# Performance work log

Measured on AMD Instinct MI355X. Metric: run time of the kernel, lower is better.

The kernel has to match this reference:

```python
import jax, jax.numpy as jnp
import numpy as np

N_HEADS = 16
N_KV_HEADS = 4
WINDOW = 128
THETA = 10000.0


def _rope_cos_sin(T, half):
    inv = 1.0 / (THETA ** (jnp.arange(half, dtype=jnp.float32) / half))
    f = jnp.arange(T, dtype=jnp.float32)[:, None] * inv[None, :]  # (T, half)
    return jnp.cos(f), jnp.sin(f)


def _apply_rope(x, cos, sin):
    # x: (B, H, T, hd); interleaved (real, imag) pairs like torch view_as_complex
    xr, xi = x[..., 0::2], x[..., 1::2]
    out_r = xr * cos - xi * sin
    out_i = xr * sin + xi * cos
    return jnp.stack([out_r, out_i], axis=-1).reshape(x.shape)


def setup_inputs() -> dict:
    key = jax.random.key(0)
    ks = jax.random.split(key, 6)
    B, T, C = 1, 4096, 2048
    kvC = (C // N_HEADS) * N_KV_HEADS
    return {
        "x": jax.random.normal(ks[0], (B, T, C), dtype=jnp.float32),
        "wq": jax.random.normal(ks[1], (C, C), dtype=jnp.float32) * 0.02,
        "wk": jax.random.normal(ks[2], (C, kvC), dtype=jnp.float32) * 0.02,
        "wv": jax.random.normal(ks[3], (C, kvC), dtype=jnp.float32) * 0.02,
        "wo": jax.random.normal(ks[4], (C, C), dtype=jnp.float32) * 0.02,
        "sink": jnp.zeros((1, N_HEADS, 1, 1), dtype=jnp.float32),
    }


def reference(x, wq, wk, wv, wo, sink):
    B, T, C = x.shape
    hd = C // N_HEADS
    n_rep = N_HEADS // N_KV_HEADS

    q = (x @ wq).reshape(B, T, N_HEADS, hd).transpose(0, 2, 1, 3)    # (B,H,T,hd)
    k = (x @ wk).reshape(B, T, N_KV_HEADS, hd).transpose(0, 2, 1, 3)  # (B,Hkv,T,hd)
    v = (x @ wv).reshape(B, T, N_KV_HEADS, hd).transpose(0, 2, 1, 3)

    cos, sin = _rope_cos_sin(T, hd // 2)  # (T, hd/2), broadcasts over (B,H,T,hd/2)
    q = _apply_rope(q, cos, sin)
    k = _apply_rope(k, cos, sin)

    # GQA head expansion (repeat_interleave over head dim)
    k = jnp.repeat(k, n_rep, axis=1)
    v = jnp.repeat(v, n_rep, axis=1)

    att = jnp.einsum("bhqd,bhkd->bhqk", q, k) * (hd ** -0.5) + sink

    # symmetric sliding-window band: |i - j| <= window//2
    idx = jnp.arange(T)
    band = jnp.abs(idx[:, None] - idx[None, :]) <= (WINDOW // 2)
    att = jnp.where(band[None, None, :, :], att, -jnp.inf)

    att = jax.nn.softmax(att, axis=-1)
    # torch code replaces NaN rows (fully-masked) with uniform; band always has diag so no-op
    att = jnp.where(jnp.isnan(att), 1.0 / T, att)

    out = jnp.einsum("bhqk,bhkd->bqhd", att, v).reshape(B, T, C)
    return out @ wo
```

## Files before the change

### kernel.cpp

```cpp
#include <hip/hip_runtime.h>
#include <stdint.h>

#define T_SEQ 4096
#define C_DIM 2048
#define HD 128

typedef unsigned short ushort_t;
typedef __attribute__((ext_vector_type(8))) short shortx8;
typedef __attribute__((ext_vector_type(4))) float floatx4;
typedef __attribute__((ext_vector_type(8))) unsigned short u16x8;
typedef __attribute__((ext_vector_type(4))) unsigned short u16x4;

__device__ __forceinline__ ushort_t f2bf(float f) {
  union { float f; uint32_t u; } v; v.f = f;
  v.u += 0x7fffu + ((v.u >> 16) & 1u);
  return (ushort_t)(v.u >> 16);
}
__device__ __forceinline__ void load_lds16(const ushort_t* g, ushort_t* l) {
  __builtin_amdgcn_global_load_lds(
      (const __attribute__((address_space(1))) unsigned int*)g,
      (__attribute__((address_space(3))) unsigned int*)l, 16, 0, 0);
}

__global__ __launch_bounds__(256) void prep_kernel(
    const float* __restrict__ wq, const float* __restrict__ wk,
    const float* __restrict__ wv, const float* __restrict__ wo,
    const float* __restrict__ x,
    ushort_t* __restrict__ BtAll, ushort_t* __restrict__ woT,
    ushort_t* __restrict__ xb) {
  const int bid = blockIdx.x;
  const int tid = threadIdx.x;
  if (bid >= 2560) {
    int i = (bid - 2560) * 256 + tid;
    float4 v = ((const float4*)x)[i];
    u16x4 o; o[0] = f2bf(v.x); o[1] = f2bf(v.y); o[2] = f2bf(v.z); o[3] = f2bf(v.w);
    ((u16x4*)xb)[i] = o;
    return;
  }
  const float* src; ushort_t* dst; int C, bx, by;
  if (bid < 1024) { src = wq; dst = BtAll; C = 2048; bx = bid & 31; by = bid >> 5; }
  else if (bid < 1280) { int b = bid - 1024; src = wk; dst = BtAll + (size_t)2048 * 2048; C = 512; bx = b & 7; by = b >> 3; }
  else if (bid < 1536) { int b = bid - 1280; src = wv; dst = BtAll + (size_t)2560 * 2048; C = 512; bx = b & 7; by = b >> 3; }
  else { int b = bid - 1536; src = wo; dst = woT; C = 2048; bx = b & 31; by = b >> 5; }
  const int R = 2048;

  __shared__ float tile[64][65];
  const int c0 = bx * 64, r0 = by * 64;
  for (int i = tid; i < 1024; i += 256) {
    int r = i >> 4, cc = (i & 15) * 4;
    float4 v = *(const float4*)&src[(size_t)(r0 + r) * C + c0 + cc];
    tile[r][cc] = v.x; tile[r][cc + 1] = v.y; tile[r][cc + 2] = v.z; tile[r][cc + 3] = v.w;
  }
  __syncthreads();
  for (int i = tid; i < 512; i += 256) {
    int oc = i >> 3;
    int g = (i & 7) * 8;
    u16x8 o;
    for (int j = 0; j < 8; ++j) o[j] = f2bf(tile[g + j][oc]);
    *(u16x8*)&dst[(size_t)(c0 + oc) * R + r0 + g] = o;
  }
}

struct GemmAcc { floatx4 a[4][4]; };

__device__ __forceinline__ void gemm_core_bk64(
    const ushort_t* __restrict__ A, const ushort_t* __restrict__ Bt,
    ushort_t* As, ushort_t* Bs, GemmAcc& acc,
    int m0, int n0, int K, int tid, int lane, int wave, int quad, int l16,
    int wm, int wn) {
  const int nk = K >> 6;
  for (int kk = 0; kk < nk; ++kk) {
    const int k0 = kk << 6;
    for (int r = 0; r < 4; ++r) {
      int e = r * 256 + tid;
      int row = e >> 3;
      int p = e & 7;
      int g = (p - row) & 7;
      const ushort_t* ga = A + (size_t)(m0 + row) * K + k0 + g * 8;
      const ushort_t* gb = Bt + (size_t)(n0 + row) * K + k0 + g * 8;
      ushort_t* la = As + (size_t)(r * 256 + (tid & 192)) * 8;
      ushort_t* lb = Bs + (size_t)(r * 256 + (tid & 192)) * 8;
      load_lds16(ga, la);
      load_lds16(gb, lb);
    }
    __syncthreads();
    for (int ks = 0; ks < 2; ++ks) {
      shortx8 af[4], bfr[4];
      for (int i = 0; i < 4; ++i) {
        int ar = wm + i * 16 + l16;
        af[i] = *(const shortx8*)(As + ar * 64 + (((ks << 2) + quad + ar) & 7) * 8);
        int br = wn + i * 16 + l16;
        bfr[i] = *(const shortx8*)(Bs + br * 64 + (((ks << 2) + quad + br) & 7) * 8);
      }
      for (int i = 0; i < 4; ++i)
        for (int j = 0; j < 4; ++j)
          acc.a[i][j] = __builtin_amdgcn_mfma_f32_16x16x32_bf16(af[i], bfr[j], acc.a[i][j], 0, 0, 0);
    }
    __syncthreads();
  }
}

__global__ __launch_bounds__(256, 3) void gemm_bf16(
    const ushort_t* __restrict__ A, const ushort_t* __restrict__ Bt,
    float* __restrict__ C, int M, int N, int K) {
  __shared__ __align__(16) ushort_t As[128 * 64];
  __shared__ __align__(16) ushort_t Bs[128 * 64];
  const int tid = threadIdx.x;
  const int lane = tid & 63;
  const int wave = tid >> 6;
  const int quad = lane >> 4;
  const int l16 = lane & 15;
  const int m0 = blockIdx.y * 128;
  const int n0 = blockIdx.x * 128;
  const int wm = (wave & 1) * 64;
  const int wn = (wave >> 1) * 64;

  GemmAcc acc = {};
  gemm_core_bk64(A, Bt, As, Bs, acc, m0, n0, K, tid, lane, wave, quad, l16, wm, wn);

  for (int i = 0; i < 4; ++i)
    for (int j = 0; j < 4; ++j) {
      int col = n0 + wn + j * 16 + l16;
      int rbase = m0 + wm + i * 16 + quad * 4;
      for (int r = 0; r < 4; ++r)
        C[(size_t)(rbase + r) * N + col] = acc.a[i][j][r];
    }
}

#define BARF() do { __builtin_amdgcn_s_barrier(); asm volatile("" ::: "memory"); } while (0)

__global__ __launch_bounds__(512, 2) void gemm_qkv256(
    const ushort_t* __restrict__ A, const ushort_t* __restrict__ Bt,
    ushort_t* __restrict__ qbb, ushort_t* __restrict__ kbb,
    ushort_t* __restrict__ vtb) {
  __shared__ __align__(16) ushort_t SA[2][16384];
  __shared__ __align__(16) ushort_t SB[2][16384];
  const int tid = threadIdx.x;
  const int lane = tid & 63;
  const int w = tid >> 6;
  const int l16 = lane & 15;
  const int quad = lane >> 4;
  const int wm = (w >> 2) * 128;
  const int wn = (w & 3) * 64;
  const int aq = wm + (w & 3) * 16;
  const int bq = wn + (w >> 2) * 16;
  const int gl8 = lane >> 3;
  const int gch = ((lane & 7) - gl8) & 7;

  const int bid = blockIdx.x;
  const int swz = (bid & 7) * 24 + (bid >> 3);
  const int n0 = (swz % 12) * 256;
  const int m0 = (swz / 12) * 256;

  const int off0 = l16 * 64 + ((quad + l16) & 7) * 8;
  const int off1 = l16 * 64 + ((4 + quad + l16) & 7) * 8;

  floatx4 acc[8][4] = {};
  shortx8 a0k0[4], a0k1[4], a1k0[4], a1k1[4];
  shortx8 b0k0[2], b0k1[2], b1k0[2], b1k1[2];

  auto issue2 = [&](const ushort_t* __restrict__ G, int gRow, ushort_t* L, int r0, int k0) {
#pragma unroll
    for (int u = 0; u < 2; ++u) {
      const ushort_t* src = G + (size_t)(gRow + r0 + u * 8 + gl8) * 2048 + k0 + gch * 8;
      load_lds16(src, L + (r0 + u * 8) * 64);
    }
  };

#define LOAD_A(base, Sb, D0, D1)                                  \
  _Pragma("unroll")                                               \
  for (int i2 = 0; i2 < 4; ++i2) {                                \
    const int rb = (wm + ((base) + i2) * 16) * 64;                \
    D0[i2] = *(const shortx8*)&(Sb)[rb + off0];                   \
    D1[i2] = *(const shortx8*)&(Sb)[rb + off1];                   \
  }
#define LOAD_B(jb, Sb, D0, D1)                                    \
  _Pragma("unroll")                                               \
  for (int j2 = 0; j2 < 2; ++j2) {                                \
    const int rb = (wn + ((jb) + j2) * 16) * 64;                  \
    D0[j2] = *(const shortx8*)&(Sb)[rb + off0];                   \
    D1[j2] = *(const shortx8*)&(Sb)[rb + off1];                   \
  }
#define MFMA16(ih, jh, A0, A1, B0, B1)                            \
  __builtin_amdgcn_s_setprio(1);                                  \
  _Pragma("unroll")                                               \
  for (int i2 = 0; i2 < 4; ++i2)                                  \
    _Pragma("unroll")                                             \
    for (int j2 = 0; j2 < 2; ++j2) {                              \
      acc[(ih)*4+i2][(jh)*2+j2] = __builtin_amdgcn_mfma_f32_16x16x32_bf16( \
          A0[i2], B0[j2], acc[(ih)*4+i2][(jh)*2+j2], 0, 0, 0);    \
      acc[(ih)*4+i2][(jh)*2+j2] = __builtin_amdgcn_mfma_f32_16x16x32_bf16( \
          A1[i2], B1[j2], acc[(ih)*4+i2][(jh)*2+j2], 0, 0, 0);    \
    }                                                             \
  __builtin_amdgcn_s_setprio(0);

  issue2(A, m0, SA[0], aq, 0);        issue2(A, m0, SA[0], aq + 64, 0);
  issue2(Bt, n0, SB[0], bq, 0);       issue2(Bt, n0, SB[0], bq + 32, 0);
  issue2(A, m0, SA[1], aq + 64, 64);  issue2(Bt, n0, SB[1], bq + 32, 64);
  asm volatile("s_waitcnt vmcnt(4)" ::: "memory");
  BARF();

  for (int t2 = 0; t2 < 16; ++t2) {
#pragma unroll
    for (int half = 0; half < 2; ++half) {
      const int t = t2 * 2 + half;
      ushort_t* SAb = SA[half];
      ushort_t* SBb = SB[half];
      ushort_t* SAo = SA[half ^ 1];
      ushort_t* SBo = SB[half ^ 1];

      LOAD_A(0, SAb, a0k0, a0k1);
      LOAD_B(0, SBb, b0k0, b0k1);
      LOAD_B(2, SBb, b1k0, b1k1);
      if (t + 1 < 32) issue2(A, m0, SAo, aq, (t + 1) * 64);
      BARF();
      MFMA16(0, 0, a0k0, a0k1, b0k0, b0k1);
      BARF();

      LOAD_A(4, SAb, a1k0, a1k1);
      if (t + 1 < 32) issue2(Bt, n0, SBo, bq, (t + 1) * 64);
      BARF();
      MFMA16(0, 1, a0k0, a0k1, b1k0, b1k1);
      BARF();

      if (t + 2 < 32) issue2(Bt, n0, SBb, bq + 32, (t + 2) * 64);
      BARF();
      MFMA16(1, 1, a1k0, a1k1, b1k0, b1k1);
      BARF();

      if (t + 2 < 32) issue2(A, m0, SAb, aq + 64, (t + 2) * 64);
      BARF();
      MFMA16(1, 0, a1k0, a1k1, b0k0, b0k1);
      if (t < 30)       { asm volatile("s_waitcnt vmcnt(4)" ::: "memory"); }
      else if (t == 30) { asm volatile("s_waitcnt vmcnt(0)" ::: "memory"); }
      BARF();
    }
  }

  asm volatile("s_waitcnt vmcnt(0) lgkmcnt(0)" ::: "memory");
  BARF();

  if (n0 < 2560) {
    const bool isq = (n0 < 2048);
    const int par = l16 & 1;
#pragma unroll
    for (int j = 0; j < 4; ++j) {
      int col = n0 + wn + j * 16 + l16;
      int irot = (col & 127) >> 1;
      float inv = __expf(-0.14391157f * (float)irot);
#pragma unroll
      for (int i = 0; i < 8; ++i) {
        int t0r = m0 + wm + i * 16 + quad * 4;
#pragma unroll
        for (int r = 0; r < 4; ++r) {
          float val = acc[i][j][r];
          float other = __shfl_xor(val, 1, 64);
          float sn, cs;
          __sincosf((float)(t0r + r) * inv, &sn, &cs);
          float outv = par ? (other * sn + val * cs) : (val * cs - other * sn);
          if (isq) qbb[(size_t)(t0r + r) * 2048 + col] = f2bf(outv);
          else     kbb[(size_t)(t0r + r) * 512 + (col - 2048)] = f2bf(outv);
        }
      }
    }
  } else {
#pragma unroll
    for (int j = 0; j < 4; ++j) {
      int dim = n0 + wn + j * 16 + l16 - 2560;
#pragma unroll
      for (int i = 0; i < 8; ++i) {
        int t0r = m0 + wm + i * 16 + quad * 4;
        u16x4 o;
#pragma unroll
        for (int r = 0; r < 4; ++r) o[r] = f2bf(acc[i][j][r]);
        *(u16x4*)&vtb[(size_t)dim * T_SEQ + t0r] = o;
      }
    }
  }
#undef LOAD_A
#undef LOAD_B
#undef MFMA16
}

#define LSTR 168
__global__ __launch_bounds__(512, 1) void attn_kernel(
    const ushort_t* __restrict__ qbb, const ushort_t* __restrict__ kbb,
    const ushort_t* __restrict__ vtb, ushort_t* __restrict__ ao) {
  __shared__ __align__(16) ushort_t QP[128 * LSTR];
  __shared__ __align__(16) ushort_t KV[160 * LSTR];

  const int tid = threadIdx.x;
  const int lane = tid & 63;
  const int wave = tid >> 6;
  const int l16 = lane & 15;
  const int quad = lane >> 4;
  const int kvh = blockIdx.x;
  const int h0 = kvh * 4;
  const int t0 = blockIdx.y * 32;
  const int kstart = t0 - 64;
  const int hsel = wave & 3;
  const int qh = wave >> 2;
  const float scale = 0.08838834764831845f;

  for (int c = tid; c < 2048; c += 512) {
    int row = c >> 4, c8 = c & 15;
    int h = h0 + (row >> 5);
    int q = t0 + (row & 31);
    u16x8 v = *(const u16x8*)&qbb[(size_t)q * C_DIM + h * HD + c8 * 8];
    *(u16x8*)&QP[row * LSTR + c8 * 8] = v;
  }
  for (int c = tid; c < 2560; c += 512) {
    int row = c >> 4, c8 = c & 15;
    int t = kstart + row;
    u16x8 v;
    if (t >= 0 && t < T_SEQ) {
      v = *(const u16x8*)&kbb[(size_t)t * 512 + kvh * HD + c8 * 8];
    } else {
      for (int z = 0; z < 8; ++z) v[z] = 0;
    }
    *(u16x8*)&KV[row * LSTR + c8 * 8] = v;
  }
  __syncthreads();

  floatx4 acc[10] = {};
  const int arow = hsel * 32 + qh * 16 + l16;
  for (int ks = 0; ks < 4; ++ks) {
    shortx8 af = *(const shortx8*)&QP[arow * LSTR + ks * 32 + quad * 8];
    for (int kt = 0; kt < 10; ++kt) {
      shortx8 bf = *(const shortx8*)&KV[(kt * 16 + l16) * LSTR + ks * 32 + quad * 8];
      acc[kt] = __builtin_amdgcn_mfma_f32_16x16x32_bf16(af, bf, acc[kt], 0, 0, 0);
    }
  }

  float mrow[4] = {-3e38f, -3e38f, -3e38f, -3e38f};
  for (int kt = 0; kt < 10; ++kt) {
    int col = kt * 16 + l16;
    int kg = kstart + col;
    for (int r = 0; r < 4; ++r) {
      int row = qh * 16 + quad * 4 + r;
      bool valid = (kg >= 0) && (kg < T_SEQ) && (col >= row) && (col <= row + 128);
      float s = valid ? acc[kt][r] * scale : -3e38f;
      acc[kt][r] = s;
      mrow[r] = fmaxf(mrow[r], s);
    }
  }
  for (int off = 1; off < 16; off <<= 1)
    for (int r = 0; r < 4; ++r)
      mrow[r] = fmaxf(mrow[r], __shfl_xor(mrow[r], off, 64));
  float rl[4];
  for (int r = 0; r < 4; ++r) {
    float s = 0.f;
    for (int kt = 0; kt < 10; ++kt) {
      float p = __expf(acc[kt][r] - mrow[r]);
      acc[kt][r] = p;
      s += p;
    }
    rl[r] = s;
  }
  for (int off = 1; off < 16; off <<= 1)
    for (int r = 0; r < 4; ++r) rl[r] += __shfl_xor(rl[r], off, 64);
  for (int r = 0; r < 4; ++r) rl[r] = 1.0f / rl[r];

  __syncthreads();

  for (int kt = 0; kt < 10; ++kt) {
    int col = kt * 16 + l16;
    for (int r = 0; r < 4; ++r) {
      int row = hsel * 32 + qh * 16 + quad * 4 + r;
      QP[row * LSTR + col] = f2bf(acc[kt][r] * rl[r]);
    }
  }
  for (int c = tid; c < 2560; c += 512) {
    int dim = c / 20, c8 = c % 20;
    int k0 = kstart + c8 * 8;
    const ushort_t* g = &vtb[(size_t)(kvh * HD + dim) * T_SEQ];
    u16x8 v;
    if (k0 >= 0 && k0 + 7 < T_SEQ) {
      v = *(const u16x8*)&g[k0];
    } else {
      for (int z = 0; z < 8; ++z) {
        int kk = k0 + z;
        v[z] = (kk >= 0 && kk < T_SEQ) ? g[kk] : (ushort_t)0;
      }
    }
    *(u16x8*)&KV[dim * LSTR + c8 * 8] = v;
  }
  __syncthreads();

  floatx4 oacc[8] = {};
  const int prow = hsel * 32 + qh * 16 + l16;
  for (int ks = 0; ks < 5; ++ks) {
    shortx8 pf = *(const shortx8*)&QP[prow * LSTR + ks * 32 + quad * 8];
    for (int dt = 0; dt < 8; ++dt) {
      shortx8 vf = *(const shortx8*)&KV[(dt * 16 + l16) * LSTR + ks * 32 + quad * 8];
      oacc[dt] = __builtin_amdgcn_mfma_f32_16x16x32_bf16(pf, vf, oacc[dt], 0, 0, 0);
    }
  }

  const int h = h0 + hsel;
  for (int r = 0; r < 4; ++r) {
    int row = t0 + qh * 16 + quad * 4 + r;
    for (int dt = 0; dt < 8; ++dt) {
      int dim = dt * 16 + l16;
      ao[(size_t)row * C_DIM + h * HD + dim] = f2bf(oacc[dt][r]);
    }
  }
}

extern "C" void kernel_launch(void* const* d_in, const int* in_sizes, int n_in,
                              void* d_out, int out_size, void* d_ws, size_t ws_size,
                              hipStream_t stream) {
  const float* x  = (const float*)d_in[0];
  const float* wq = (const float*)d_in[1];
  const float* wk = (const float*)d_in[2];
  const float* wv = (const float*)d_in[3];
  const float* wo = (const float*)d_in[4];
  float* out = (float*)d_out;

  char* ws = (char*)d_ws;
  ushort_t* BtAll = (ushort_t*)(ws);
  ushort_t* woT   = (ushort_t*)(ws + 12582912);
  ushort_t* xb    = (ushort_t*)(ws + 20971520);
  ushort_t* qbb   = (ushort_t*)(ws + 37748736);
  ushort_t* kbb   = (ushort_t*)(ws + 54525952);
  ushort_t* vtb   = (ushort_t*)(ws + 58720256);
  ushort_t* ao    = (ushort_t*)(ws + 62914560);

  prep_kernel<<<10752, 256, 0, stream>>>(wq, wk, wv, wo, x, BtAll, woT, xb);

  gemm_qkv256<<<192, 512, 0, stream>>>(xb, BtAll, qbb, kbb, vtb);

  attn_kernel<<<dim3(4, 128), 512, 0, stream>>>(qbb, kbb, vtb, ao);

  gemm_bf16<<<dim3(16, 32), 256, 0, stream>>>(ao, woT, out, 4096, 2048, 2048);
}
```

Baseline: 256.6 us.

## Double query tile per attention block to reuse K/V window loads

The attention kernel now handles 64 query positions per block instead of 32. Each wave processes two 16-row query sub-tiles against a 208-row K/V window, and the grid is halved. The intent is to cut redundant loads of the overlapping K/V window, since the 128-key halo is amortized over twice as many queries. This costs more LDS, more registers per wave from the doubled accumulators, and fewer blocks for parallelism. The QKV GEMM's launch bound minimum-blocks hint also changes from 2 to 1, which may loosen register limits.

```diff
diff --git a/kernel.cpp b/kernel.cpp
--- a/kernel.cpp
+++ b/kernel.cpp
@@ -129,7 +129,7 @@
 
 #define BARF() do { __builtin_amdgcn_s_barrier(); asm volatile("" ::: "memory"); } while (0)
 
-__global__ __launch_bounds__(512, 2) void gemm_qkv256(
+__global__ __launch_bounds__(512, 1) void gemm_qkv256(
     const ushort_t* __restrict__ A, const ushort_t* __restrict__ Bt,
     ushort_t* __restrict__ qbb, ushort_t* __restrict__ kbb,
     ushort_t* __restrict__ vtb) {
@@ -282,12 +282,14 @@
 #undef MFMA16
 }
 
-#define LSTR 168
+#define QSTR 168
+#define KSTR 168
+#define VSTR 216
 __global__ __launch_bounds__(512, 1) void attn_kernel(
     const ushort_t* __restrict__ qbb, const ushort_t* __restrict__ kbb,
     const ushort_t* __restrict__ vtb, ushort_t* __restrict__ ao) {
-  __shared__ __align__(16) ushort_t QP[128 * LSTR];
-  __shared__ __align__(16) ushort_t KV[160 * LSTR];
+  __shared__ __align__(16) ushort_t QP[256 * QSTR];
+  __shared__ __align__(16) ushort_t KV[208 * KSTR];
 
   const int tid = threadIdx.x;
   const int lane = tid & 63;
@@ -296,20 +298,20 @@
   const int quad = lane >> 4;
   const int kvh = blockIdx.x;
   const int h0 = kvh * 4;
-  const int t0 = blockIdx.y * 32;
+  const int t0 = blockIdx.y * 64;
   const int kstart = t0 - 64;
   const int hsel = wave & 3;
   const int qh = wave >> 2;
   const float scale = 0.08838834764831845f;
 
-  for (int c = tid; c < 2048; c += 512) {
+  for (int c = tid; c < 4096; c += 512) {
     int row = c >> 4, c8 = c & 15;
-    int h = h0 + (row >> 5);
-    int q = t0 + (row & 31);
+    int h = h0 + (row >> 6);
+    int q = t0 + (row & 63);
     u16x8 v = *(const u16x8*)&qbb[(size_t)q * C_DIM + h * HD + c8 * 8];
-    *(u16x8*)&QP[row * LSTR + c8 * 8] = v;
-  }
-  for (int c = tid; c < 2560; c += 512) {
+    *(u16x8*)&QP[row * QSTR + c8 * 8] = v;
+  }
+  for (int c = tid; c < 3328; c += 512) {
     int row = c >> 4, c8 = c & 15;
     int t = kstart + row;
     u16x8 v;
@@ -318,60 +320,77 @@
     } else {
       for (int z = 0; z < 8; ++z) v[z] = 0;
     }
-    *(u16x8*)&KV[row * LSTR + c8 * 8] = v;
+    *(u16x8*)&KV[row * KSTR + c8 * 8] = v;
   }
   __syncthreads();
 
-  floatx4 acc[10] = {};
-  const int arow = hsel * 32 + qh * 16 + l16;
+  const int qb0 = qh * 32, qb1 = qb0 + 16;
+  const int tb0 = qb0 >> 4, tb1 = tb0 + 1;
+  floatx4 acc0[10] = {}, acc1[10] = {};
   for (int ks = 0; ks < 4; ++ks) {
-    shortx8 af = *(const shortx8*)&QP[arow * LSTR + ks * 32 + quad * 8];
+    shortx8 af0 = *(const shortx8*)&QP[(hsel * 64 + qb0 + l16) * QSTR + ks * 32 + quad * 8];
+    shortx8 af1 = *(const shortx8*)&QP[(hsel * 64 + qb1 + l16) * QSTR + ks * 32 + quad * 8];
     for (int kt = 0; kt < 10; ++kt) {
-      shortx8 bf = *(const shortx8*)&KV[(kt * 16 + l16) * LSTR + ks * 32 + quad * 8];
-      acc[kt] = __builtin_amdgcn_mfma_f32_16x16x32_bf16(af, bf, acc[kt], 0, 0, 0);
-    }
-  }
-
-  float mrow[4] = {-3e38f, -3e38f, -3e38f, -3e38f};
-  for (int kt = 0; kt < 10; ++kt) {
-    int col = kt * 16 + l16;
-    int kg = kstart + col;
+      shortx8 bf0 = *(const shortx8*)&KV[((tb0 + kt) * 16 + l16) * KSTR + ks * 32 + quad * 8];
+      acc0[kt] = __builtin_amdgcn_mfma_f32_16x16x32_bf16(af0, bf0, acc0[kt], 0, 0, 0);
+      shortx8 bf1 = *(const shortx8*)&KV[((tb1 + kt) * 16 + l16) * KSTR + ks * 32 + quad * 8];
+      acc1[kt] = __builtin_amdgcn_mfma_f32_16x16x32_bf16(af1, bf1, acc1[kt], 0, 0, 0);
+    }
+  }
+
+  float rl0[4], rl1[4];
+#pragma unroll
+  for (int s = 0; s < 2; ++s) {
+    floatx4* acc = s ? acc1 : acc0;
+    const int qb = s ? qb1 : qb0;
+    const int tb = s ? tb1 : tb0;
+    float* rl = s ? rl1 : rl0;
+    float mrow[4] = {-3e38f, -3e38f, -3e38f, -3e38f};
+    for (int kt = 0; kt < 10; ++kt) {
+      int col = (tb + kt) * 16 + l16;
+      int kg = kstart + col;
+      for (int r = 0; r < 4; ++r) {
+        int qrow = qb + quad * 4 + r;
+        bool valid = (kg >= 0) && (kg < T_SEQ) && (col >= qrow) && (col <= qrow + 128);
+        float sc = valid ? acc[kt][r] * scale : -3e38f;
+        acc[kt][r] = sc;
+        mrow[r] = fmaxf(mrow[r], sc);
+      }
+    }
+    for (int off = 1; off < 16; off <<= 1)
+      for (int r = 0; r < 4; ++r)
+        mrow[r] = fmaxf(mrow[r], __shfl_xor(mrow[r], off, 64));
     for (int r = 0; r < 4; ++r) {
-      int row = qh * 16 + quad * 4 + r;
-      bool valid = (kg >= 0) && (kg < T_SEQ) && (col >= row) && (col <= row + 128);
-      float s = valid ? acc[kt][r] * scale : -3e38f;
-      acc[kt][r] = s;
-      mrow[r] = fmaxf(mrow[r], s);
-    }
-  }
-  for (int off = 1; off < 16; off <<= 1)
-    for (int r = 0; r < 4; ++r)
-      mrow[r] = fmaxf(mrow[r], __shfl_xor(mrow[r], off, 64));
-  float rl[4];
-  for (int r = 0; r < 4; ++r) {
-    float s = 0.f;
+      float ss = 0.f;
+      for (int kt = 0; kt < 10; ++kt) {
+        float p = __expf(acc[kt][r] - mrow[r]);
+        acc[kt][r] = p;
+        ss += p;
+      }
+      rl[r] = ss;
+    }
+    for (int off = 1; off < 16; off <<= 1)
+      for (int r = 0; r < 4; ++r) rl[r] += __shfl_xor(rl[r], off, 64);
+    for (int r = 0; r < 4; ++r) rl[r] = 1.0f / rl[r];
+  }
+
+  __syncthreads();
+
+#pragma unroll
+  for (int s = 0; s < 2; ++s) {
+    floatx4* acc = s ? acc1 : acc0;
+    const int qb = s ? qb1 : qb0;
+    float* rl = s ? rl1 : rl0;
     for (int kt = 0; kt < 10; ++kt) {
-      float p = __expf(acc[kt][r] - mrow[r]);
-      acc[kt][r] = p;
-      s += p;
-    }
-    rl[r] = s;
-  }
-  for (int off = 1; off < 16; off <<= 1)
-    for (int r = 0; r < 4; ++r) rl[r] += __shfl_xor(rl[r], off, 64);
-  for (int r = 0; r < 4; ++r) rl[r] = 1.0f / rl[r];
-
-  __syncthreads();
-
-  for (int kt = 0; kt < 10; ++kt) {
-    int col = kt * 16 + l16;
-    for (int r = 0; r < 4; ++r) {
-      int row = hsel * 32 + qh * 16 + quad * 4 + r;
-      QP[row * LSTR + col] = f2bf(acc[kt][r] * rl[r]);
-    }
-  }
-  for (int c = tid; c < 2560; c += 512) {
-    int dim = c / 20, c8 = c % 20;
+      int col = kt * 16 + l16;
+      for (int r = 0; r < 4; ++r) {
+        int row = hsel * 64 + qb + quad * 4 + r;
+        QP[row * QSTR + col] = f2bf(acc[kt][r] * rl[r]);
+      }
+    }
+  }
+  for (int c = tid; c < 3328; c += 512) {
+    int dim = c / 26, c8 = c % 26;
     int k0 = kstart + c8 * 8;
     const ushort_t* g = &vtb[(size_t)(kvh * HD + dim) * T_SEQ];
     u16x8 v;
@@ -383,26 +402,29 @@
         v[z] = (kk >= 0 && kk < T_SEQ) ? g[kk] : (ushort_t)0;
       }
     }
-    *(u16x8*)&KV[dim * LSTR + c8 * 8] = v;
+    *(u16x8*)&KV[dim * VSTR + c8 * 8] = v;
   }
   __syncthreads();
 
-  floatx4 oacc[8] = {};
-  const int prow = hsel * 32 + qh * 16 + l16;
-  for (int ks = 0; ks < 5; ++ks) {
-    shortx8 pf = *(const shortx8*)&QP[prow * LSTR + ks * 32 + quad * 8];
-    for (int dt = 0; dt < 8; ++dt) {
-      shortx8 vf = *(const shortx8*)&KV[(dt * 16 + l16) * LSTR + ks * 32 + quad * 8];
-      oacc[dt] = __builtin_amdgcn_mfma_f32_16x16x32_bf16(pf, vf, oacc[dt], 0, 0, 0);
-    }
-  }
-
-  const int h = h0 + hsel;
-  for (int r = 0; r < 4; ++r) {
-    int row = t0 + qh * 16 + quad * 4 + r;
-    for (int dt = 0; dt < 8; ++dt) {
-      int dim = dt * 16 + l16;
-      ao[(size_t)row * C_DIM + h * HD + dim] = f2bf(oacc[dt][r]);
+#pragma unroll
+  for (int s = 0; s < 2; ++s) {
+    const int qb = s ? qb1 : qb0;
+    const int prow = hsel * 64 + qb + l16;
+    floatx4 oacc[8] = {};
+    for (int ks = 0; ks < 5; ++ks) {
+      shortx8 pf = *(const shortx8*)&QP[prow * QSTR + ks * 32 + quad * 8];
+      for (int dt = 0; dt < 8; ++dt) {
+        shortx8 vf = *(const shortx8*)&KV[(dt * 16 + l16) * VSTR + qb + ks * 32 + quad * 8];
+        oacc[dt] = __builtin_amdgcn_mfma_f32_16x16x32_bf16(pf, vf, oacc[dt], 0, 0, 0);
+      }
+    }
+    const int h = h0 + hsel;
+    for (int r = 0; r < 4; ++r) {
+      int row = t0 + qb + quad * 4 + r;
+      for (int dt = 0; dt < 8; ++dt) {
+        int dim = dt * 16 + l16;
+        ao[(size_t)row * C_DIM + h * HD + dim] = f2bf(oacc[dt][r]);
+      }
     }
   }
 }
@@ -430,7 +452,7 @@
 
   gemm_qkv256<<<192, 512, 0, stream>>>(xb, BtAll, qbb, kbb, vtb);
 
-  attn_kernel<<<dim3(4, 128), 512, 0, stream>>>(qbb, kbb, vtb, ao);
+  attn_kernel<<<dim3(4, 64), 512, 0, stream>>>(qbb, kbb, vtb, ao);
 
   gemm_bf16<<<dim3(16, 32), 256, 0, stream>>>(ao, woT, out, 4096, 2048, 2048);
 }
```

Measured after the change: 255.8 us. About the same (-0.3%).
